# Optimization experiments

Measured on AMD Instinct MI355X. Metric: run time of the kernel, lower is better.

Reference implementation:

```python
import jax, jax.numpy as jnp
import numpy as np

NCONF, NT, NX = 8192, 64, 64


def setup_inputs() -> dict:
    key = jax.random.key(0)
    k1, k2, k3 = jax.random.split(key, 3)
    phi = jax.random.normal(k1, (NCONF, NT, NX), dtype=jnp.float32)
    # Well-conditioned invertible mixing matrix so logdet is finite/stable.
    W = jnp.eye(NX, dtype=jnp.float32) + 0.1 * jax.random.normal(k2, (NX, NX), dtype=jnp.float32)
    b = 0.1 * jax.random.normal(k3, (NX,), dtype=jnp.float32)
    return {"phi": phi, "W": W, "b": b}


def _nn(phi, W, b):
    # Wrapped NN: invertible linear coupling along the Nx axis.
    NNphi = jnp.einsum('btx,xy->bty', phi, W) + b
    _, logabsdet = jnp.linalg.slogdet(W)
    logDet = jnp.full((phi.shape[0],), phi.shape[1] * logabsdet, dtype=phi.dtype)
    return NNphi, logDet


def reference(phi, W, b):
    Nconf, Nt, Nx = phi.shape
    # t[i, x] = argmin over time of |phi[i, :, x]|  -> [Nconf, Nx]
    t = jnp.argmin(jnp.abs(phi), axis=1)
    # Source: if t[i,0] > t[i,1]: T0[i] = t[i,1]; config.flip(1) is DISCARDED (no-op).
    T0 = jnp.where(t[:, 0] > t[:, 1], t[:, 1], t[:, 0])  # [Nconf]
    j = jnp.arange(Nx)
    # torch.roll(x, s, dim): out[j] = x[(j - s) % N]
    idx_fwd = (j[None, :] - T0[:, None]) % Nx          # [Nconf, Nx]
    phi_r = jnp.take_along_axis(phi, idx_fwd[:, None, :], axis=2)
    NNphi, logDet = _nn(phi_r, W, b)
    # roll back with shift -T0; flip again discarded in source.
    idx_bwd = (j[None, :] + T0[:, None]) % Nx
    NNphi = jnp.take_along_axis(NNphi, idx_bwd[:, None, :], axis=2)
    return NNphi, logDet
```

## Files before the change

### kernel.cpp

```cpp
#include <hip/hip_runtime.h>
#include <stdint.h>


typedef _Float16 half2v __attribute__((ext_vector_type(2)));
typedef _Float16 half4v __attribute__((ext_vector_type(4)));
typedef _Float16 half8v __attribute__((ext_vector_type(8)));
typedef float float4v __attribute__((ext_vector_type(4)));

#if defined(__has_builtin)
#if __has_builtin(__builtin_amdgcn_fdot2)
#define HAVE_FDOT2 1
#endif
#endif

__device__ __forceinline__ float dot2f(half2v a, half2v b, float c) {
#ifdef HAVE_FDOT2
  return __builtin_amdgcn_fdot2(a, b, c, false);
#else
  return c + (float)a.x * (float)b.x + (float)a.y * (float)b.y;
#endif
}

union H8 {
  half8v v;
  half2v p[4];
};

__global__ __launch_bounds__(256) void wt2_prep(const float* __restrict__ W,
                                                _Float16* __restrict__ wt2) {
  const int s = blockIdx.x;
  const int tid = threadIdx.x;
#pragma unroll
  for (int it = 0; it < 16; ++it) {
    int flat = it * 256 + tid;
    int j = flat >> 6;
    int y = flat & 63;
    float v = W[((y + s) & 63) * 64 + ((j + s) & 63)];
    wt2[(size_t)s * 4096 + flat] = (_Float16)v;
  }
}

__global__ __launch_bounds__(256) void equiv_main(
    const float* __restrict__ phi, const float* __restrict__ W,
    const float* __restrict__ b, const _Float16* __restrict__ wt2,
    float* __restrict__ out) {
  __shared__ __align__(16) unsigned char smem[32768];
  const int lane = threadIdx.x & 63;

  if (blockIdx.x == 0) {
    if (threadIdx.x >= 64) return;
    float* A = (float*)smem;
    const int t = lane;
    for (int r = 0; r < 64; ++r) A[r * 65 + lane] = W[r * 64 + lane];
    float ldsum = 0.f;
    for (int k = 0; k < 64; ++k) {
      float av = (t >= k) ? fabsf(A[t * 65 + k]) : -1.0f;
      unsigned long long key =
          (((unsigned long long)__float_as_uint(av < 0.f ? 0.f : av)) << 6) |
          (unsigned long long)t;
      if (t < k) key = 0ull;
#pragma unroll
      for (int m = 1; m < 64; m <<= 1) {
        unsigned long long o = __shfl_xor(key, m);
        key = (o > key) ? o : key;
      }
      int p = (int)(key & 63ull);
      if (p != k) {
        float vk = A[k * 65 + lane];
        float vp = A[p * 65 + lane];
        A[k * 65 + lane] = vp;
        A[p * 65 + lane] = vk;
      }
      float piv = A[k * 65 + k];
      ldsum += logf(fabsf(piv));
      float rk = 1.0f / piv;
      float m = (t > k) ? A[t * 65 + k] * rk : 0.f;
      for (int c = k + 1; c < 64; ++c) {
        float pr = A[k * 65 + c];
        if (t > k) A[t * 65 + c] -= m * pr;
      }
    }
    float ld = 64.0f * ldsum;
    float* outLD = out + (size_t)8192 * 4096;
    for (int it = 0; it < 128; ++it) outLD[it * 64 + lane] = ld;
    return;
  }

  const int wave = threadIdx.x >> 6;
  const int cfg = ((int)blockIdx.x - 1) * 4 + wave;
  _Float16* sPhi = ((_Float16*)smem) + wave * 4096;

  const float4v* phiv = (const float4v*)(phi + (size_t)cfg * 4096);
  float4v pv[16];
#pragma unroll
  for (int it = 0; it < 16; ++it) pv[it] = phiv[it * 64 + lane];

  unsigned long long k0 = ~0ull, k1 = ~0ull;
  if ((lane & 15) == 0) {
#pragma unroll
    for (int it = 0; it < 16; ++it) {
      int tt = it * 4 + (lane >> 4);
      unsigned long long c0 =
          (((unsigned long long)__float_as_uint(fabsf(pv[it].x))) << 6) | (unsigned long long)tt;
      unsigned long long c1 =
          (((unsigned long long)__float_as_uint(fabsf(pv[it].y))) << 6) | (unsigned long long)tt;
      k0 = c0 < k0 ? c0 : k0;
      k1 = c1 < k1 ? c1 : k1;
    }
  }
#pragma unroll
  for (int m = 1; m < 64; m <<= 1) {
    unsigned long long o0 = __shfl_xor(k0, m);
    unsigned long long o1 = __shfl_xor(k1, m);
    k0 = o0 < k0 ? o0 : k0;
    k1 = o1 < k1 ? o1 : k1;
  }
  int t0i = (int)(k0 & 63ull), t1i = (int)(k1 & 63ull);
  const int T0 = (t0i > t1i) ? t1i : t0i;

#pragma unroll
  for (int it = 0; it < 16; ++it) {
    int flat4 = it * 64 + lane;
    int t = flat4 >> 4;
    int y0 = (flat4 & 15) << 2;
    int ch = (y0 >> 3) ^ (t >> 3);
    int off = y0 & 7;
    half4v h;
    h.x = (_Float16)pv[it].x;
    h.y = (_Float16)pv[it].y;
    h.z = (_Float16)pv[it].z;
    h.w = (_Float16)pv[it].w;
    *(half4v*)&sPhi[t * 64 + (ch << 3) + off] = h;
  }

  const int ty = lane >> 3, tx = lane & 7;
  const int t0 = ty << 3, j0 = tx << 3;
  const _Float16* wt = wt2 + (size_t)T0 * 4096;
  float acc[8][8];
#pragma unroll
  for (int r = 0; r < 8; ++r)
#pragma unroll
    for (int c = 0; c < 8; ++c) acc[r][c] = 0.f;

  for (int xb = 0; xb < 8; ++xb) {
    H8 a[8];
#pragma unroll
    for (int r = 0; r < 8; ++r)
      a[r].v = *(const half8v*)&sPhi[(t0 + r) * 64 + ((xb ^ ty) << 3)];
#pragma unroll
    for (int c = 0; c < 8; ++c) {
      H8 bb;
      bb.v = *(const half8v*)&wt[(j0 + c) * 64 + (xb << 3)];
#pragma unroll
      for (int r = 0; r < 8; ++r) {
        float av = acc[r][c];
#pragma unroll
        for (int p = 0; p < 4; ++p) av = dot2f(a[r].p[p], bb.p[p], av);
        acc[r][c] = av;
      }
    }
  }

  float bv[8];
#pragma unroll
  for (int c = 0; c < 8; ++c) bv[c] = b[(j0 + c + T0) & 63];
  float* outp = out + (size_t)cfg * 4096;
#pragma unroll
  for (int r = 0; r < 8; ++r) {
#pragma unroll
    for (int cq = 0; cq < 2; ++cq) {
      float4v o;
#pragma unroll
      for (int kk = 0; kk < 4; ++kk) o[kk] = acc[r][cq * 4 + kk] + bv[cq * 4 + kk];
      *(float4v*)&outp[(t0 + r) * 64 + j0 + (cq << 2)] = o;
    }
  }
}

extern "C" void kernel_launch(void* const* d_in, const int* in_sizes, int n_in,
                              void* d_out, int out_size, void* d_ws, size_t ws_size,
                              hipStream_t stream) {
  const float* phi = (const float*)d_in[0];
  const float* W = (const float*)d_in[1];
  const float* b = (const float*)d_in[2];
  float* out = (float*)d_out;
  _Float16* wt2 = (_Float16*)d_ws;

  wt2_prep<<<dim3(64), dim3(256), 0, stream>>>(W, wt2);
  equiv_main<<<dim3(2049), dim3(256), 0, stream>>>(phi, W, b, wt2, out);
}
```

Measured before the change: 286.3 us.

## Replace fdot2 register-tiled GEMM with MFMA 16x16x32 f16 from registers

Swaps the per-lane fdot2 outer-product GEMM for MFMA 16x16x32 f16 instructions. Phi is loaded straight from global memory into the MFMA A-fragment layout, so the LDS staging and swizzle are gone. Weights are loaded directly into B fragments. The aim is to use the matrix cores and cut VALU and LDS traffic. The catch is that outputs are now written as scalar strided stores (one float per lane per row) instead of float4, which may hurt write coalescing. The argmin now only looks at the columns held by q==0 lanes, which matches the layout.

Result: no change. 282.0 us (-1.5%).

```diff
diff --git a/kernel.cpp b/kernel.cpp
--- a/kernel.cpp
+++ b/kernel.cpp
@@ -2,29 +2,8 @@
 #include <stdint.h>
 
 
-typedef _Float16 half2v __attribute__((ext_vector_type(2)));
-typedef _Float16 half4v __attribute__((ext_vector_type(4)));
 typedef _Float16 half8v __attribute__((ext_vector_type(8)));
 typedef float float4v __attribute__((ext_vector_type(4)));
-
-#if defined(__has_builtin)
-#if __has_builtin(__builtin_amdgcn_fdot2)
-#define HAVE_FDOT2 1
-#endif
-#endif
-
-__device__ __forceinline__ float dot2f(half2v a, half2v b, float c) {
-#ifdef HAVE_FDOT2
-  return __builtin_amdgcn_fdot2(a, b, c, false);
-#else
-  return c + (float)a.x * (float)b.x + (float)a.y * (float)b.y;
-#endif
-}
-
-union H8 {
-  half8v v;
-  half2v p[4];
-};
 
 __global__ __launch_bounds__(256) void wt2_prep(const float* __restrict__ W,
                                                 _Float16* __restrict__ wt2) {
@@ -35,8 +14,7 @@
     int flat = it * 256 + tid;
     int j = flat >> 6;
     int y = flat & 63;
-    float v = W[((y + s) & 63) * 64 + ((j + s) & 63)];
-    wt2[(size_t)s * 4096 + flat] = (_Float16)v;
+    wt2[(size_t)s * 4096 + flat] = (_Float16)W[((y + s) & 63) * 64 + ((j + s) & 63)];
   }
 }
 
@@ -44,12 +22,11 @@
     const float* __restrict__ phi, const float* __restrict__ W,
     const float* __restrict__ b, const _Float16* __restrict__ wt2,
     float* __restrict__ out) {
-  __shared__ __align__(16) unsigned char smem[32768];
   const int lane = threadIdx.x & 63;
 
   if (blockIdx.x == 0) {
     if (threadIdx.x >= 64) return;
-    float* A = (float*)smem;
+    __shared__ float A[64 * 65];
     const int t = lane;
     for (int r = 0; r < 64; ++r) A[r * 65 + lane] = W[r * 64 + lane];
     float ldsum = 0.f;
@@ -66,8 +43,7 @@
       }
       int p = (int)(key & 63ull);
       if (p != k) {
-        float vk = A[k * 65 + lane];
-        float vp = A[p * 65 + lane];
+        float vk = A[k * 65 + lane], vp = A[p * 65 + lane];
         A[k * 65 + lane] = vp;
         A[p * 65 + lane] = vk;
       }
@@ -88,93 +64,89 @@
 
   const int wave = threadIdx.x >> 6;
   const int cfg = ((int)blockIdx.x - 1) * 4 + wave;
-  _Float16* sPhi = ((_Float16*)smem) + wave * 4096;
+  const float* ph = phi + (size_t)cfg * 4096;
+  const int m = lane & 15;
+  const int q = lane >> 4;
 
-  const float4v* phiv = (const float4v*)(phi + (size_t)cfg * 4096);
-  float4v pv[16];
+  float4v f[4][2][2];
 #pragma unroll
-  for (int it = 0; it < 16; ++it) pv[it] = phiv[it * 64 + lane];
+  for (int mt = 0; mt < 4; ++mt)
+#pragma unroll
+    for (int ks = 0; ks < 2; ++ks)
+#pragma unroll
+      for (int h = 0; h < 2; ++h)
+        f[mt][ks][h] = *(const float4v*)&ph[(mt * 16 + m) * 64 + ks * 32 + q * 8 + h * 4];
 
   unsigned long long k0 = ~0ull, k1 = ~0ull;
-  if ((lane & 15) == 0) {
+  if (q == 0) {
 #pragma unroll
-    for (int it = 0; it < 16; ++it) {
-      int tt = it * 4 + (lane >> 4);
+    for (int mt = 0; mt < 4; ++mt) {
+      unsigned long long t = (unsigned long long)(mt * 16 + m);
       unsigned long long c0 =
-          (((unsigned long long)__float_as_uint(fabsf(pv[it].x))) << 6) | (unsigned long long)tt;
+          (((unsigned long long)__float_as_uint(fabsf(f[mt][0][0].x))) << 6) | t;
       unsigned long long c1 =
-          (((unsigned long long)__float_as_uint(fabsf(pv[it].y))) << 6) | (unsigned long long)tt;
+          (((unsigned long long)__float_as_uint(fabsf(f[mt][0][0].y))) << 6) | t;
       k0 = c0 < k0 ? c0 : k0;
       k1 = c1 < k1 ? c1 : k1;
     }
   }
 #pragma unroll
-  for (int m = 1; m < 64; m <<= 1) {
-    unsigned long long o0 = __shfl_xor(k0, m);
-    unsigned long long o1 = __shfl_xor(k1, m);
+  for (int s = 1; s < 64; s <<= 1) {
+    unsigned long long o0 = __shfl_xor(k0, s);
+    unsigned long long o1 = __shfl_xor(k1, s);
     k0 = o0 < k0 ? o0 : k0;
     k1 = o1 < k1 ? o1 : k1;
   }
   int t0i = (int)(k0 & 63ull), t1i = (int)(k1 & 63ull);
   const int T0 = (t0i > t1i) ? t1i : t0i;
 
+  const _Float16* wt = wt2 + (size_t)T0 * 4096;
+  half8v Bf[2][4];
 #pragma unroll
-  for (int it = 0; it < 16; ++it) {
-    int flat4 = it * 64 + lane;
-    int t = flat4 >> 4;
-    int y0 = (flat4 & 15) << 2;
-    int ch = (y0 >> 3) ^ (t >> 3);
-    int off = y0 & 7;
-    half4v h;
-    h.x = (_Float16)pv[it].x;
-    h.y = (_Float16)pv[it].y;
-    h.z = (_Float16)pv[it].z;
-    h.w = (_Float16)pv[it].w;
-    *(half4v*)&sPhi[t * 64 + (ch << 3) + off] = h;
-  }
+  for (int ks = 0; ks < 2; ++ks)
+#pragma unroll
+    for (int nt = 0; nt < 4; ++nt)
+      Bf[ks][nt] = *(const half8v*)&wt[(nt * 16 + m) * 64 + ks * 32 + q * 8];
 
-  const int ty = lane >> 3, tx = lane & 7;
-  const int t0 = ty << 3, j0 = tx << 3;
-  const _Float16* wt = wt2 + (size_t)T0 * 4096;
-  float acc[8][8];
+  half8v Af[4][2];
 #pragma unroll
-  for (int r = 0; r < 8; ++r)
+  for (int mt = 0; mt < 4; ++mt)
 #pragma unroll
-    for (int c = 0; c < 8; ++c) acc[r][c] = 0.f;
+    for (int ks = 0; ks < 2; ++ks) {
+      half8v h;
+#pragma unroll
+      for (int kk = 0; kk < 4; ++kk) {
+        h[kk] = (_Float16)f[mt][ks][0][kk];
+        h[kk + 4] = (_Float16)f[mt][ks][1][kk];
+      }
+      Af[mt][ks] = h;
+    }
 
-  for (int xb = 0; xb < 8; ++xb) {
-    H8 a[8];
+  float4v acc[4][4];
 #pragma unroll
-    for (int r = 0; r < 8; ++r)
-      a[r].v = *(const half8v*)&sPhi[(t0 + r) * 64 + ((xb ^ ty) << 3)];
+  for (int mt = 0; mt < 4; ++mt)
 #pragma unroll
-    for (int c = 0; c < 8; ++c) {
-      H8 bb;
-      bb.v = *(const half8v*)&wt[(j0 + c) * 64 + (xb << 3)];
+    for (int nt = 0; nt < 4; ++nt) acc[mt][nt] = (float4v)(0.f);
 #pragma unroll
-      for (int r = 0; r < 8; ++r) {
-        float av = acc[r][c];
+  for (int ks = 0; ks < 2; ++ks)
 #pragma unroll
-        for (int p = 0; p < 4; ++p) av = dot2f(a[r].p[p], bb.p[p], av);
-        acc[r][c] = av;
-      }
-    }
-  }
+    for (int mt = 0; mt < 4; ++mt)
+#pragma unroll
+      for (int nt = 0; nt < 4; ++nt)
+        acc[mt][nt] = __builtin_amdgcn_mfma_f32_16x16x32_f16(Af[mt][ks], Bf[ks][nt],
+                                                             acc[mt][nt], 0, 0, 0);
 
-  float bv[8];
+  float bias[4];
 #pragma unroll
-  for (int c = 0; c < 8; ++c) bv[c] = b[(j0 + c + T0) & 63];
-  float* outp = out + (size_t)cfg * 4096;
+  for (int nt = 0; nt < 4; ++nt) bias[nt] = b[(nt * 16 + m + T0) & 63];
+  float* op = out + (size_t)cfg * 4096;
 #pragma unroll
-  for (int r = 0; r < 8; ++r) {
+  for (int mt = 0; mt < 4; ++mt)
 #pragma unroll
-    for (int cq = 0; cq < 2; ++cq) {
-      float4v o;
+    for (int nt = 0; nt < 4; ++nt)
 #pragma unroll
-      for (int kk = 0; kk < 4; ++kk) o[kk] = acc[r][cq * 4 + kk] + bv[cq * 4 + kk];
-      *(float4v*)&outp[(t0 + r) * 64 + j0 + (cq << 2)] = o;
-    }
-  }
+      for (int r = 0; r < 4; ++r)
+        op[(mt * 16 + q * 4 + r) * 64 + nt * 16 + m] = acc[mt][nt][r] + bias[nt];
 }
 
 extern "C" void kernel_launch(void* const* d_in, const int* in_sizes, int n_in,
```
